# Performance work log

Hardware: AMD Instinct MI355X
Metric: run time of the kernel (lower is better)

The kernel has to match this reference:

```python
import jax, jax.numpy as jnp
import numpy as np

N_NODES = 50000
N_EDGES = 400000
F_IN = 16
F_OUT = 32
S_EDGE = 4


def setup_inputs() -> dict:
    key = jax.random.key(0)
    ks = jax.random.split(key, 8)
    x = jax.random.normal(ks[0], (N_NODES, F_IN), dtype=jnp.float32)
    edge_index = jax.random.randint(ks[1], (2, N_EDGES), 0, N_NODES, dtype=jnp.int64)
    edge_attr = jax.random.uniform(ks[2], (N_EDGES, S_EDGE), dtype=jnp.float32)
    # filter-generating network: single linear layer S -> F_IN*F_OUT (spektral default)
    W_kn = jax.random.normal(ks[3], (S_EDGE, F_IN * F_OUT), dtype=jnp.float32) * (1.0 / np.sqrt(S_EDGE))
    b_kn = jnp.zeros((F_IN * F_OUT,), dtype=jnp.float32)
    W_root = jax.random.normal(ks[4], (F_IN, F_OUT), dtype=jnp.float32) * (1.0 / np.sqrt(F_IN))
    b_conv = jnp.zeros((F_OUT,), dtype=jnp.float32)
    W_dense = jax.random.normal(ks[5], (F_OUT, 3), dtype=jnp.float32) * (1.0 / np.sqrt(F_OUT))
    b_dense = jnp.zeros((3,), dtype=jnp.float32)
    return {"x": x, "edge_index": edge_index, "edge_attr": edge_attr,
            "W_kn": W_kn, "b_kn": b_kn, "W_root": W_root, "b_conv": b_conv,
            "W_dense": W_dense, "b_dense": b_dense}


def reference(x, edge_index, edge_attr, W_kn, b_kn, W_root, b_conv, W_dense, b_dense):
    tgt = edge_index[0]  # aggregate into these nodes
    src = edge_index[1]  # neighbors we gather from
    # per-edge filter matrices: [E, F_IN, F_OUT]
    filt = (edge_attr @ W_kn + b_kn).reshape(-1, F_IN, F_OUT)
    # gather neighbor features and apply edge-conditioned filter: [E, F_OUT]
    msg = jnp.einsum('ef,efh->eh', x[src], filt)
    # scatter-sum aggregation to target nodes: [N, F_OUT]
    agg = jax.ops.segment_sum(msg, tgt, num_segments=N_NODES)
    # root (self) transform + bias, no activation (ECCConv default)
    h = agg + x @ W_root + b_conv
    # Dropout(0.5) is identity at inference. GlobalSumPool over nodes -> [1, F_OUT]
    pooled = jnp.sum(h, axis=0, keepdims=True)
    # Dense(3, relu)
    return jax.nn.relu(pooled @ W_dense + b_dense)
```

## Files before the change

kernel.cpp:

```cpp
#include <hip/hip_runtime.h>


#define F_IN 16
#define F_OUT 32
#define EDGE_BLOCKS 128
#define X_BLOCKS 32
#define THREADS 256

__global__ void zero_ws(float* __restrict__ ws) {
    int t = threadIdx.x;
    if (t < 96) ws[t] = 0.0f;
}

__global__ __launch_bounds__(THREADS) void reduce_kernel(
    const float* __restrict__ x, const int* __restrict__ ei,
    const float* __restrict__ ea, float* __restrict__ ws, int N, int E) {
    __shared__ float lred[4][96];
    const int bid  = blockIdx.x;
    const int tid  = threadIdx.x;
    const int wave = tid >> 6;
    const int lane = tid & 63;

    if (bid < EDGE_BLOCKS) {
        float acc[80];
        #pragma unroll
        for (int i = 0; i < 80; ++i) acc[i] = 0.0f;

        const int gtid   = bid * THREADS + tid;
        const int stride = EDGE_BLOCKS * THREADS;
        for (int e = gtid; e < E; e += stride) {
            const int s = ei[(size_t)E + e];
            const float4 a = *reinterpret_cast<const float4*>(ea + (size_t)e * 4);
            const float4* xr = reinterpret_cast<const float4*>(x + (size_t)s * 16);
            float4 v0 = xr[0], v1 = xr[1], v2 = xr[2], v3 = xr[3];
            float xs[16];
            xs[0]=v0.x; xs[1]=v0.y; xs[2]=v0.z; xs[3]=v0.w;
            xs[4]=v1.x; xs[5]=v1.y; xs[6]=v1.z; xs[7]=v1.w;
            xs[8]=v2.x; xs[9]=v2.y; xs[10]=v2.z; xs[11]=v2.w;
            xs[12]=v3.x; xs[13]=v3.y; xs[14]=v3.z; xs[15]=v3.w;
            #pragma unroll
            for (int f = 0; f < 16; ++f) {
                const float v = xs[f];
                acc[64 + f] += v;
                acc[f*4+0] = fmaf(v, a.x, acc[f*4+0]);
                acc[f*4+1] = fmaf(v, a.y, acc[f*4+1]);
                acc[f*4+2] = fmaf(v, a.z, acc[f*4+2]);
                acc[f*4+3] = fmaf(v, a.w, acc[f*4+3]);
            }
        }
        #pragma unroll
        for (int i = 0; i < 80; ++i) {
            float v = acc[i];
            #pragma unroll
            for (int m = 1; m < 64; m <<= 1) v += __shfl_xor(v, m, 64);
            if (lane == 0) lred[wave][i] = v;
        }
        __syncthreads();
        if (tid < 80) {
            float v = lred[0][tid] + lred[1][tid] + lred[2][tid] + lred[3][tid];
            atomicAdd(&ws[tid], v);
        }
    } else {
        float cs[16];
        #pragma unroll
        for (int i = 0; i < 16; ++i) cs[i] = 0.0f;

        const int gtid   = (bid - EDGE_BLOCKS) * THREADS + tid;
        const int stride = X_BLOCKS * THREADS;
        for (int r = gtid; r < N; r += stride) {
            const float4* xr = reinterpret_cast<const float4*>(x + (size_t)r * 16);
            float4 v0 = xr[0], v1 = xr[1], v2 = xr[2], v3 = xr[3];
            cs[0]+=v0.x; cs[1]+=v0.y; cs[2]+=v0.z;  cs[3]+=v0.w;
            cs[4]+=v1.x; cs[5]+=v1.y; cs[6]+=v1.z;  cs[7]+=v1.w;
            cs[8]+=v2.x; cs[9]+=v2.y; cs[10]+=v2.z; cs[11]+=v2.w;
            cs[12]+=v3.x; cs[13]+=v3.y; cs[14]+=v3.z; cs[15]+=v3.w;
        }
        #pragma unroll
        for (int i = 0; i < 16; ++i) {
            float v = cs[i];
            #pragma unroll
            for (int m = 1; m < 64; m <<= 1) v += __shfl_xor(v, m, 64);
            if (lane == 0) lred[wave][i] = v;
        }
        __syncthreads();
        if (tid < 16) {
            float v = lred[0][tid] + lred[1][tid] + lred[2][tid] + lred[3][tid];
            atomicAdd(&ws[80 + tid], v);
        }
    }
}

__global__ void finalize(
    const float* __restrict__ ws,
    const float* __restrict__ W_kn, const float* __restrict__ b_kn,
    const float* __restrict__ W_root, const float* __restrict__ b_conv,
    const float* __restrict__ W_dense, const float* __restrict__ b_dense,
    float* __restrict__ out, int N) {
    __shared__ float pooled[32];
    const int t = threadIdx.x;
    if (t < 32) {
        float p = (float)N * b_conv[t];
        #pragma unroll
        for (int f = 0; f < 16; ++f) {
            float tsum = 0.0f;
            #pragma unroll
            for (int s = 0; s < 4; ++s)
                tsum = fmaf(ws[f*4+s], W_kn[s*512 + f*32 + t], tsum);
            p += tsum;
            p = fmaf(ws[64+f], b_kn[f*32+t], p);
            p = fmaf(ws[80+f], W_root[f*32+t], p);
        }
        pooled[t] = p;
    }
    __syncthreads();
    if (t < 3) {
        float o = b_dense[t];
        #pragma unroll
        for (int h = 0; h < 32; ++h) o = fmaf(pooled[h], W_dense[h*3+t], o);
        out[t] = fmaxf(o, 0.0f);
    }
}

extern "C" void kernel_launch(void* const* d_in, const int* in_sizes, int n_in,
                              void* d_out, int out_size, void* d_ws, size_t ws_size,
                              hipStream_t stream) {
    const float* x       = (const float*)d_in[0];
    const int*   ei      = (const int*)d_in[1];
    const float* ea      = (const float*)d_in[2];
    const float* W_kn    = (const float*)d_in[3];
    const float* b_kn    = (const float*)d_in[4];
    const float* W_root  = (const float*)d_in[5];
    const float* b_conv  = (const float*)d_in[6];
    const float* W_dense = (const float*)d_in[7];
    const float* b_dense = (const float*)d_in[8];
    float* ws  = (float*)d_ws;
    float* out = (float*)d_out;

    const int N = in_sizes[0] / F_IN;
    const int E = in_sizes[1] / 2;

    hipLaunchKernelGGL(zero_ws, dim3(1), dim3(96), 0, stream, ws);
    hipLaunchKernelGGL(reduce_kernel, dim3(EDGE_BLOCKS + X_BLOCKS), dim3(THREADS),
                       0, stream, x, ei, ea, ws, N, E);
    hipLaunchKernelGGL(finalize, dim3(1), dim3(64), 0, stream,
                       ws, W_kn, b_kn, W_root, b_conv, W_dense, b_dense, out, N);
}
```

Baseline: 104.7 us.

## Replace global atomics with per-block slots and use transpose-style wave reduction

Drops the zero-init kernel by writing each block's partial sums to its own workspace slot, which the final kernel then reduces serially. The per-wave butterfly reduction of 80 accumulators is replaced by a recursive-halving exchange that splits the vectors across lanes, cutting shuffle count from 480 to about 90 per wave. It uses shared-memory atomics to combine waves, and the block size doubles to 512. The cost is a serial 128-element loop per thread in the final single-block kernel.

Measured after the change: 89.35 us. 14.7% less time.

```diff
diff --git a/kernel.cpp b/kernel.cpp
--- a/kernel.cpp
+++ b/kernel.cpp
@@ -2,24 +2,23 @@
 
 
 #define F_IN 16
-#define F_OUT 32
 #define EDGE_BLOCKS 128
 #define X_BLOCKS 32
-#define THREADS 256
+#define TOTAL_BLOCKS (EDGE_BLOCKS + X_BLOCKS)
+#define THREADS 512
 
-__global__ void zero_ws(float* __restrict__ ws) {
-    int t = threadIdx.x;
-    if (t < 96) ws[t] = 0.0f;
-}
-
-__global__ __launch_bounds__(THREADS) void reduce_kernel(
+__global__ __launch_bounds__(THREADS) void partial_kernel(
     const float* __restrict__ x, const int* __restrict__ ei,
     const float* __restrict__ ea, float* __restrict__ ws, int N, int E) {
-    __shared__ float lred[4][96];
+    __shared__ float lred[96];
     const int bid  = blockIdx.x;
     const int tid  = threadIdx.x;
-    const int wave = tid >> 6;
     const int lane = tid & 63;
+    const bool b5 = (lane & 32) != 0, b4 = (lane & 16) != 0;
+    const bool b3 = (lane & 8)  != 0, b2 = (lane & 4)  != 0;
+
+    if (tid < 96) lred[tid] = 0.0f;
+    __syncthreads();
 
     if (bid < EDGE_BLOCKS) {
         float acc[80];
@@ -32,12 +31,9 @@
             const int s = ei[(size_t)E + e];
             const float4 a = *reinterpret_cast<const float4*>(ea + (size_t)e * 4);
             const float4* xr = reinterpret_cast<const float4*>(x + (size_t)s * 16);
-            float4 v0 = xr[0], v1 = xr[1], v2 = xr[2], v3 = xr[3];
-            float xs[16];
-            xs[0]=v0.x; xs[1]=v0.y; xs[2]=v0.z; xs[3]=v0.w;
-            xs[4]=v1.x; xs[5]=v1.y; xs[6]=v1.z; xs[7]=v1.w;
-            xs[8]=v2.x; xs[9]=v2.y; xs[10]=v2.z; xs[11]=v2.w;
-            xs[12]=v3.x; xs[13]=v3.y; xs[14]=v3.z; xs[15]=v3.w;
+            const float4 v0 = xr[0], v1 = xr[1], v2 = xr[2], v3 = xr[3];
+            const float xs[16] = {v0.x,v0.y,v0.z,v0.w, v1.x,v1.y,v1.z,v1.w,
+                                  v2.x,v2.y,v2.z,v2.w, v3.x,v3.y,v3.z,v3.w};
             #pragma unroll
             for (int f = 0; f < 16; ++f) {
                 const float v = xs[f];
@@ -48,18 +44,43 @@
                 acc[f*4+3] = fmaf(v, a.w, acc[f*4+3]);
             }
         }
+
         #pragma unroll
-        for (int i = 0; i < 80; ++i) {
-            float v = acc[i];
+        for (int i = 0; i < 40; ++i) {
+            const float sendv = b5 ? acc[i] : acc[i+40];
+            const float keepv = b5 ? acc[i+40] : acc[i];
+            acc[i] = keepv + __shfl_xor(sendv, 32, 64);
+        }
+        #pragma unroll
+        for (int i = 0; i < 20; ++i) {
+            const float sendv = b4 ? acc[i] : acc[i+20];
+            const float keepv = b4 ? acc[i+20] : acc[i];
+            acc[i] = keepv + __shfl_xor(sendv, 16, 64);
+        }
+        #pragma unroll
+        for (int i = 0; i < 10; ++i) {
+            const float sendv = b3 ? acc[i] : acc[i+10];
+            const float keepv = b3 ? acc[i+10] : acc[i];
+            acc[i] = keepv + __shfl_xor(sendv, 8, 64);
+        }
+        #pragma unroll
+        for (int i = 0; i < 5; ++i) {
+            const float sendv = b2 ? acc[i] : acc[i+5];
+            const float keepv = b2 ? acc[i+5] : acc[i];
+            acc[i] = keepv + __shfl_xor(sendv, 4, 64);
+        }
+        #pragma unroll
+        for (int i = 0; i < 5; ++i) {
+            acc[i] += __shfl_xor(acc[i], 2, 64);
+            acc[i] += __shfl_xor(acc[i], 1, 64);
+        }
+        if ((lane & 3) == 0) {
+            const int vbase = (b5?40:0) + (b4?20:0) + (b3?10:0) + (b2?5:0);
             #pragma unroll
-            for (int m = 1; m < 64; m <<= 1) v += __shfl_xor(v, m, 64);
-            if (lane == 0) lred[wave][i] = v;
+            for (int i = 0; i < 5; ++i) atomicAdd(&lred[vbase + i], acc[i]);
         }
         __syncthreads();
-        if (tid < 80) {
-            float v = lred[0][tid] + lred[1][tid] + lred[2][tid] + lred[3][tid];
-            atomicAdd(&ws[tid], v);
-        }
+        if (tid < 80) ws[(size_t)bid * 96 + tid] = lred[tid];
     } else {
         float cs[16];
         #pragma unroll
@@ -69,35 +90,62 @@
         const int stride = X_BLOCKS * THREADS;
         for (int r = gtid; r < N; r += stride) {
             const float4* xr = reinterpret_cast<const float4*>(x + (size_t)r * 16);
-            float4 v0 = xr[0], v1 = xr[1], v2 = xr[2], v3 = xr[3];
+            const float4 v0 = xr[0], v1 = xr[1], v2 = xr[2], v3 = xr[3];
             cs[0]+=v0.x; cs[1]+=v0.y; cs[2]+=v0.z;  cs[3]+=v0.w;
             cs[4]+=v1.x; cs[5]+=v1.y; cs[6]+=v1.z;  cs[7]+=v1.w;
             cs[8]+=v2.x; cs[9]+=v2.y; cs[10]+=v2.z; cs[11]+=v2.w;
             cs[12]+=v3.x; cs[13]+=v3.y; cs[14]+=v3.z; cs[15]+=v3.w;
         }
         #pragma unroll
-        for (int i = 0; i < 16; ++i) {
-            float v = cs[i];
-            #pragma unroll
-            for (int m = 1; m < 64; m <<= 1) v += __shfl_xor(v, m, 64);
-            if (lane == 0) lred[wave][i] = v;
+        for (int i = 0; i < 8; ++i) {
+            const float sendv = b5 ? cs[i] : cs[i+8];
+            const float keepv = b5 ? cs[i+8] : cs[i];
+            cs[i] = keepv + __shfl_xor(sendv, 32, 64);
         }
+        #pragma unroll
+        for (int i = 0; i < 4; ++i) {
+            const float sendv = b4 ? cs[i] : cs[i+4];
+            const float keepv = b4 ? cs[i+4] : cs[i];
+            cs[i] = keepv + __shfl_xor(sendv, 16, 64);
+        }
+        #pragma unroll
+        for (int i = 0; i < 2; ++i) {
+            const float sendv = b3 ? cs[i] : cs[i+2];
+            const float keepv = b3 ? cs[i+2] : cs[i];
+            cs[i] = keepv + __shfl_xor(sendv, 8, 64);
+        }
+        {
+            const float sendv = b2 ? cs[0] : cs[1];
+            const float keepv = b2 ? cs[1] : cs[0];
+            cs[0] = keepv + __shfl_xor(sendv, 4, 64);
+        }
+        cs[0] += __shfl_xor(cs[0], 2, 64);
+        cs[0] += __shfl_xor(cs[0], 1, 64);
+        if ((lane & 3) == 0) atomicAdd(&lred[80 + (lane >> 2)], cs[0]);
         __syncthreads();
-        if (tid < 16) {
-            float v = lred[0][tid] + lred[1][tid] + lred[2][tid] + lred[3][tid];
-            atomicAdd(&ws[80 + tid], v);
-        }
+        if (tid < 16) ws[(size_t)bid * 96 + 80 + tid] = lred[80 + tid];
     }
 }
 
-__global__ void finalize(
-    const float* __restrict__ ws,
+__global__ __launch_bounds__(128) void final_kernel(
+    const float* __restrict__ slots,
     const float* __restrict__ W_kn, const float* __restrict__ b_kn,
     const float* __restrict__ W_root, const float* __restrict__ b_conv,
     const float* __restrict__ W_dense, const float* __restrict__ b_dense,
     float* __restrict__ out, int N) {
+    __shared__ float red[96];
     __shared__ float pooled[32];
     const int t = threadIdx.x;
+    if (t < 96) {
+        float s = 0.0f;
+        if (t < 80) {
+            for (int b = 0; b < EDGE_BLOCKS; ++b) s += slots[(size_t)b * 96 + t];
+        } else {
+            for (int b = EDGE_BLOCKS; b < TOTAL_BLOCKS; ++b) s += slots[(size_t)b * 96 + t];
+        }
+        red[t] = s;
+    }
+    __syncthreads();
     if (t < 32) {
         float p = (float)N * b_conv[t];
         #pragma unroll
@@ -105,10 +153,10 @@
             float tsum = 0.0f;
             #pragma unroll
             for (int s = 0; s < 4; ++s)
-                tsum = fmaf(ws[f*4+s], W_kn[s*512 + f*32 + t], tsum);
+                tsum = fmaf(red[f*4+s], W_kn[s*512 + f*32 + t], tsum);
             p += tsum;
-            p = fmaf(ws[64+f], b_kn[f*32+t], p);
-            p = fmaf(ws[80+f], W_root[f*32+t], p);
+            p = fmaf(red[64+f], b_kn[f*32+t], p);
+            p = fmaf(red[80+f], W_root[f*32+t], p);
         }
         pooled[t] = p;
     }
@@ -139,9 +187,8 @@
     const int N = in_sizes[0] / F_IN;
     const int E = in_sizes[1] / 2;
 
-    hipLaunchKernelGGL(zero_ws, dim3(1), dim3(96), 0, stream, ws);
-    hipLaunchKernelGGL(reduce_kernel, dim3(EDGE_BLOCKS + X_BLOCKS), dim3(THREADS),
+    hipLaunchKernelGGL(partial_kernel, dim3(TOTAL_BLOCKS), dim3(THREADS),
                        0, stream, x, ei, ea, ws, N, E);
-    hipLaunchKernelGGL(finalize, dim3(1), dim3(64), 0, stream,
+    hipLaunchKernelGGL(final_kernel, dim3(1), dim3(128), 0, stream,
                        ws, W_kn, b_kn, W_root, b_conv, W_dense, b_dense, out, N);
 }
```
